# Kernel tuning notes

Measured on AMD Instinct MI355X. Metric: run time of the kernel, lower is better.

## Reference

```python
import jax, jax.numpy as jnp
import numpy as np


def setup_inputs() -> dict:
    key = jax.random.key(0)
    ks = jax.random.split(key, 15)
    B, r, d, h, na = 64, 64, 2048, 64, 256
    x = jax.random.normal(ks[0], (B, d, na), dtype=jnp.float32)
    L = jax.random.randint(ks[1], (B, 2, na), 0, 2).astype(jnp.float32)
    p = lambda i, shp: jax.random.normal(ks[i], shp, dtype=jnp.float32)
    return {
        "x": x, "L": L,
        "Aq": p(2, (r, d)), "Ak": p(3, (r, d)), "Av": p(4, (r, d)),
        "Aq1": p(5, (r, r)), "Ak1": p(6, (r, r)), "Av1": p(7, (r, r)),
        "Aq5": p(8, (r, r)), "Ak5": p(9, (r, r)), "Av5": p(10, (r, r)),
        "Ao": p(11, (r, r)), "Ao1": p(12, (r, r)), "Ao5": p(13, (h, r)),
    }


def reference(x, L, Aq, Ak, Av, Aq1, Ak1, Av1, Aq5, Ak5, Av5, Ao, Ao1, Ao5):
    B, d, na = x.shape
    # numNeighbors: count of L[:,0,:] >= 1 per batch, +1 -> [B,1,1]
    numN = jnp.sum((L[:, 0, :] >= 1.0).astype(jnp.float32), axis=1)[:, None, None] + 1.0
    scale = jnp.sqrt(numN)  # [B,1,1]

    def attn(M, Wq, Wk, Wv):
        # M: [B, f, na]; Wq/Wk/Wv: [r, f]
        Q = jax.nn.sigmoid(jnp.einsum('rf,bfn->bnr', Wq, M))  # [B,na,r]
        K = jax.nn.sigmoid(jnp.einsum('rf,bfn->brn', Wk, M))  # [B,r,na]
        V = jax.nn.sigmoid(jnp.einsum('rf,bfn->bnr', Wv, M))  # [B,na,r]
        A = jax.nn.softmax(jnp.einsum('bnr,brm->bnm', Q, K) / scale, axis=2)
        return jnp.einsum('bnm,bmr->brn', A, V)  # [B,r,na]

    o = attn(x, Aq, Ak, Av)
    M = jax.nn.silu(jnp.einsum('sr,brn->bsn', Ao, o))
    o = attn(M, Aq1, Ak1, Av1)
    M = jax.nn.silu(jnp.einsum('sr,brn->bsn', Ao1, o))
    o = attn(M, Aq5, Ak5, Av5)
    M = jax.nn.silu(jnp.einsum('hr,brn->bhn', Ao5, o))  # [B,h,na]

    blk = d // na  # rows per block (8)
    def diagvec(i):
        # kron(sum-of-squares, ones(1,2)) == repeat each element twice -> [B, 2*na]
        return jnp.repeat(jnp.sum(M[:, i * blk:(i + 1) * blk, :] ** 2, axis=1), 2, axis=1)

    M11, M12, M21, M22 = diagvec(0), diagvec(1), diagvec(2), diagvec(3)
    Mpp = jnp.sum(M[:, 4 * blk:, :] ** 2, axis=1)  # [B, na]

    # q = x[:, :4, :].transpose(1,2).reshape(B, 4*na) (agent-major ordering)
    q = jnp.transpose(x[:, :4, :], (0, 2, 1)).reshape(B, 4 * na)
    q1, q2 = q[:, :2 * na], q[:, 2 * na:]
    # Block matrix [[diag(M11), diag(M12)], [diag(M21), diag(M22)]] quadratic form,
    # computed without materializing the [B, 4na, 4na] matrix.
    quad = jnp.sum(M11 * q1 * q1 + M12 * q1 * q2 + M21 * q2 * q1 + M22 * q2 * q2,
                   axis=1, keepdims=True)
    return quad + jnp.sum(Mpp, axis=1, keepdims=True)  # [B, 1]
```

## Files before the change

### kernel.cpp

```cpp
#include <hip/hip_runtime.h>
#include <stdint.h>

typedef _Float16 f16;
typedef f16 f16x8 __attribute__((ext_vector_type(8)));
typedef float f32x4 __attribute__((ext_vector_type(4)));

#define MFMA(a,b,c) __builtin_amdgcn_mfma_f32_16x16x32_f16(a, b, c, 0, 0, 0)

__device__ __forceinline__ float sigmoidf_(float z) { return 1.0f / (1.0f + __expf(-z)); }

__global__ void prep_kernel(const float* __restrict__ L,
    const float* __restrict__ Aq, const float* __restrict__ Ak, const float* __restrict__ Av,
    const float* __restrict__ Aq1, const float* __restrict__ Ak1, const float* __restrict__ Av1,
    const float* __restrict__ Aq5, const float* __restrict__ Ak5, const float* __restrict__ Av5,
    const float* __restrict__ Ao, const float* __restrict__ Ao1, const float* __restrict__ Ao5,
    float* __restrict__ scale, f16* __restrict__ Wcat, f16* __restrict__ Wsm)
{
  __shared__ float r4[4];
  int blk = blockIdx.x, t = threadIdx.x;
  if (blk < 64) {
    float v = (L[blk * 512 + t] >= 1.0f) ? 1.0f : 0.0f;
    #pragma unroll
    for (int off = 32; off; off >>= 1) v += __shfl_down(v, off);
    if ((t & 63) == 0) r4[t >> 6] = v;
    __syncthreads();
    if (t == 0) scale[blk] = sqrtf(r4[0] + r4[1] + r4[2] + r4[3] + 1.0f);
  } else if (blk < 160) {
    int base = (blk - 64) * 4096;
    for (int i = 0; i < 16; i++) {
      int idx = base + t + i * 256;
      int row = idx >> 11, col = idx & 2047;
      float v = (row < 64) ? Aq[row * 2048 + col]
              : (row < 128) ? Ak[(row - 64) * 2048 + col]
              : Av[(row - 128) * 2048 + col];
      Wcat[idx] = (f16)v;
    }
  } else {
    int j = blk - 160;
    const float* s = (j == 0) ? Aq1 : (j == 1) ? Ak1 : (j == 2) ? Av1 : (j == 3) ? Aq5
                   : (j == 4) ? Ak5 : (j == 5) ? Av5 : (j == 6) ? Ao : (j == 7) ? Ao1 : Ao5;
    for (int i = 0; i < 16; i++) { int idx = t + i * 256; Wsm[j * 4096 + idx] = (f16)s[idx]; }
  }
}

__global__ __launch_bounds__(256) void qkv1_kernel(const float* __restrict__ x,
    const f16* __restrict__ Wcat, f16* __restrict__ Qt, f16* __restrict__ Kt,
    f16* __restrict__ Vg)
{
  int b = blockIdx.y, n0 = blockIdx.x * 64;
  int t = threadIdx.x, lane = t & 63, w = t >> 6;
  int l15 = lane & 15, q = lane >> 4;
  __shared__ f16 xt[64 * 72];
  __shared__ f16 wt[192 * 72];
  f32x4 acc[4][3] = {};
  const float* xb = x + (size_t)b * 2048 * 256 + n0;
  int tn = t & 63, fp0 = t >> 6;

  for (int f0 = 0; f0 < 2048; f0 += 64) {
    #pragma unroll
    for (int rep = 0; rep < 8; rep++) {
      int fl = (fp0 + rep * 4) * 2;
      float a0 = xb[(size_t)(f0 + fl) * 256 + tn];
      float a1 = xb[(size_t)(f0 + fl + 1) * 256 + tn];
      uint32_t pk = (uint32_t)__builtin_bit_cast(uint16_t, (f16)a0)
                  | ((uint32_t)__builtin_bit_cast(uint16_t, (f16)a1) << 16);
      *(uint32_t*)&xt[tn * 72 + fl] = pk;
    }
    #pragma unroll
    for (int i = 0; i < 6; i++) {
      int id = t + i * 256, r = id >> 3, c = id & 7;
      uint4 v = *(const uint4*)(Wcat + (size_t)r * 2048 + f0 + c * 8);
      *(uint4*)&wt[r * 72 + c * 8] = v;
    }
    __syncthreads();
    #pragma unroll
    for (int ks = 0; ks < 2; ks++) {
      int k0 = ks * 32 + q * 8;
      f16x8 af[4], bf[3];
      #pragma unroll
      for (int nt = 0; nt < 4; nt++) af[nt] = *(const f16x8*)&xt[(nt * 16 + l15) * 72 + k0];
      #pragma unroll
      for (int j = 0; j < 3; j++) bf[j] = *(const f16x8*)&wt[((w * 3 + j) * 16 + l15) * 72 + k0];
      #pragma unroll
      for (int nt = 0; nt < 4; nt++)
        #pragma unroll
        for (int j = 0; j < 3; j++)
          acc[nt][j] = MFMA(af[nt], bf[j], acc[nt][j]);
    }
    __syncthreads();
  }
  #pragma unroll
  for (int nt = 0; nt < 4; nt++)
    #pragma unroll
    for (int j = 0; j < 3; j++) {
      int rr = (w * 3 + j) * 16 + l15;
      float s[4];
      #pragma unroll
      for (int reg = 0; reg < 4; reg++) s[reg] = sigmoidf_(acc[nt][j][reg]);
      int nbase = n0 + nt * 16 + q * 4;
      if (rr < 64) {
        #pragma unroll
        for (int reg = 0; reg < 4; reg++)
          Qt[(size_t)b * 16384 + (size_t)(nbase + reg) * 64 + rr] = (f16)s[reg];
      } else if (rr < 128) {
        #pragma unroll
        for (int reg = 0; reg < 4; reg++)
          Kt[(size_t)b * 16384 + (size_t)(nbase + reg) * 64 + (rr - 64)] = (f16)s[reg];
      } else {
        union { f16 h[4]; uint2 u; } pk;
        #pragma unroll
        for (int reg = 0; reg < 4; reg++) pk.h[reg] = (f16)s[reg];
        *(uint2*)(Vg + (size_t)b * 16384 + (size_t)(rr - 128) * 256 + nbase) = pk.u;
      }
    }
}

__global__ __launch_bounds__(512) void attn_kernel(const float* __restrict__ x,
    const float* __restrict__ scale, const f16* __restrict__ Wsm,
    const f16* __restrict__ Qtg, const f16* __restrict__ Ktg, const f16* __restrict__ Vgg,
    float* __restrict__ out)
{
  int b = blockIdx.x;
  int t = threadIdx.x, lane = t & 63, w = t >> 6;
  int l15 = lane & 15, q = lane >> 4;
  __shared__ f16 S1[256 * 72];
  __shared__ f16 S2[256 * 72];
  __shared__ f16 S3[256 * 72];
  __shared__ f16 S4[256 * 72];
  __shared__ f16 S5[64 * 72];
  __shared__ float denomS[256];
  __shared__ float red[8];

  float sinv = 1.0f / scale[b];

  {
    const uint4* qs = (const uint4*)(Qtg + (size_t)b * 16384);
    const uint4* ks = (const uint4*)(Ktg + (size_t)b * 16384);
    const uint4* vs = (const uint4*)(Vgg + (size_t)b * 16384);
    #pragma unroll
    for (int i = 0; i < 4; i++) {
      int id = t + i * 512;
      int n = id >> 3, c = id & 7;
      *(uint4*)((char*)S2 + n * 144 + c * 16) = qs[id];
      *(uint4*)((char*)S3 + n * 144 + c * 16) = ks[id];
    }
    #pragma unroll
    for (int i = 0; i < 4; i++) {
      int id = t + i * 512;
      int r = id >> 5, c = id & 31;
      *(uint4*)((char*)S1 + r * 528 + c * 16) = vs[id];
    }
    if (t < 256) denomS[t] = 0.0f;
  }
  __syncthreads();

  #pragma unroll 1
  for (int l = 0; l < 3; l++) {
    if (l > 0) {
      const f16* Wq = Wsm + (size_t)((l == 1) ? 0 : 3) * 4096;
      const f16* Wk = Wsm + (size_t)((l == 1) ? 1 : 4) * 4096;
      f16x8 bq[4][2], bk[4][2];
      #pragma unroll
      for (int rt = 0; rt < 4; rt++) {
        int r = rt * 16 + l15;
        bq[rt][0] = *(const f16x8*)(Wq + r * 64 + q * 8);
        bq[rt][1] = *(const f16x8*)(Wq + r * 64 + 32 + q * 8);
        bk[rt][0] = *(const f16x8*)(Wk + r * 64 + q * 8);
        bk[rt][1] = *(const f16x8*)(Wk + r * 64 + 32 + q * 8);
      }
      #pragma unroll
      for (int half = 0; half < 2; half++) {
        int nt = 2 * w + half;
        int arow = (nt * 16 + l15) * 72;
        f16x8 af0 = *(const f16x8*)&S1[arow + q * 8];
        f16x8 af1 = *(const f16x8*)&S1[arow + 32 + q * 8];
        #pragma unroll
        for (int rt = 0; rt < 4; rt++) {
          f32x4 aq = {}; aq = MFMA(af0, bq[rt][0], aq); aq = MFMA(af1, bq[rt][1], aq);
          f32x4 akk = {}; akk = MFMA(af0, bk[rt][0], akk); akk = MFMA(af1, bk[rt][1], akk);
          int col = rt * 16 + l15;
          #pragma unroll
          for (int reg = 0; reg < 4; reg++) {
            int n = nt * 16 + q * 4 + reg;
            S2[n * 72 + col] = (f16)sigmoidf_(aq[reg]);
            S3[n * 72 + col] = (f16)sigmoidf_(akk[reg]);
          }
        }
      }
      if (t < 256) denomS[t] = 0.0f;
    }
    __syncthreads();

    f32x4 oacc[2][4] = {};
    const f16* Wv = Wsm + (size_t)((l == 1) ? 2 : 5) * 4096;

    #pragma unroll 1
    for (int ch = 0; ch < 4; ch++) {
      int m0 = ch * 64;
      if (l > 0) {
        #pragma unroll
        for (int i = 0; i < 2; i++) {
          int id = 2 * w + i, rt = id >> 2, mt = id & 3;
          int r = rt * 16 + l15;
          f16x8 a0 = *(const f16x8*)(Wv + r * 64 + q * 8);
          f16x8 a1 = *(const f16x8*)(Wv + r * 64 + 32 + q * 8);
          int brow = (m0 + mt * 16 + l15) * 72;
          f16x8 b0 = *(const f16x8*)&S1[brow + q * 8];
          f16x8 b1 = *(const f16x8*)&S1[brow + 32 + q * 8];
          f32x4 a = {}; a = MFMA(a0, b0, a); a = MFMA(a1, b1, a);
          int col = mt * 16 + l15;
          #pragma unroll
          for (int reg = 0; reg < 4; reg++)
            S5[(rt * 16 + q * 4 + reg) * 72 + col] = (f16)sigmoidf_(a[reg]);
        }
      }
      #pragma unroll
      for (int half = 0; half < 2; half++) {
        int nt = 2 * w + half;
        int arow = (nt * 16 + l15) * 72;
        f16x8 af0 = *(const f16x8*)&S2[arow + q * 8];
        f16x8 af1 = *(const f16x8*)&S2[arow + 32 + q * 8];
        #pragma unroll
        for (int mt = 0; mt < 4; mt++) {
          int brow = (m0 + mt * 16 + l15) * 72;
          f16x8 b0 = *(const f16x8*)&S3[brow + q * 8];
          f16x8 b1 = *(const f16x8*)&S3[brow + 32 + q * 8];
          f32x4 a = {}; a = MFMA(af0, b0, a); a = MFMA(af1, b1, a);
          int col = mt * 16 + l15;
          #pragma unroll
          for (int reg = 0; reg < 4; reg++) {
            float e = __expf(a[reg] * sinv);
            S4[(nt * 16 + q * 4 + reg) * 72 + col] = (f16)e;
          }
        }
      }
      __syncthreads();
      if (t < 256) {
        float s = 0.0f;
        const f16* row = &S4[t * 72];
        #pragma unroll
        for (int jj = 0; jj < 8; jj++) {
          f16x8 v = *(const f16x8*)(row + jj * 8);
          s += (float)v[0] + (float)v[1] + (float)v[2] + (float)v[3]
             + (float)v[4] + (float)v[5] + (float)v[6] + (float)v[7];
        }
        denomS[t] += s;
      }
      {
        f16x8 vb[4][2];
        #pragma unroll
        for (int rt = 0; rt < 4; rt++) {
          int r = rt * 16 + l15;
          if (l == 0) {
            vb[rt][0] = *(const f16x8*)&S1[r * 264 + m0 + q * 8];
            vb[rt][1] = *(const f16x8*)&S1[r * 264 + m0 + 32 + q * 8];
          } else {
            vb[rt][0] = *(const f16x8*)&S5[r * 72 + q * 8];
            vb[rt][1] = *(const f16x8*)&S5[r * 72 + 32 + q * 8];
          }
        }
        #pragma unroll
        for (int half = 0; half < 2; half++) {
          int nt = 2 * w + half;
          int arow = (nt * 16 + l15) * 72;
          f16x8 af0 = *(const f16x8*)&S4[arow + q * 8];
          f16x8 af1 = *(const f16x8*)&S4[arow + 32 + q * 8];
          #pragma unroll
          for (int rt = 0; rt < 4; rt++) {
            oacc[half][rt] = MFMA(af0, vb[rt][0], oacc[half][rt]);
            oacc[half][rt] = MFMA(af1, vb[rt][1], oacc[half][rt]);
          }
        }
      }
      __syncthreads();
    }

    #pragma unroll
    for (int half = 0; half < 2; half++) {
      int nt = 2 * w + half;
      #pragma unroll
      for (int rt = 0; rt < 4; rt++) {
        int col = rt * 16 + l15;
        #pragma unroll
        for (int reg = 0; reg < 4; reg++) {
          int n = nt * 16 + q * 4 + reg;
          S2[n * 72 + col] = (f16)(oacc[half][rt][reg] / denomS[n]);
        }
      }
    }
    __syncthreads();
    {
      const f16* Wo = Wsm + (size_t)((l == 0) ? 6 : (l == 1) ? 7 : 8) * 4096;
      f16x8 bo[4][2];
      #pragma unroll
      for (int st = 0; st < 4; st++) {
        int s = st * 16 + l15;
        bo[st][0] = *(const f16x8*)(Wo + s * 64 + q * 8);
        bo[st][1] = *(const f16x8*)(Wo + s * 64 + 32 + q * 8);
      }
      #pragma unroll
      for (int half = 0; half < 2; half++) {
        int nt = 2 * w + half;
        int arow = (nt * 16 + l15) * 72;
        f16x8 af0 = *(const f16x8*)&S2[arow + q * 8];
        f16x8 af1 = *(const f16x8*)&S2[arow + 32 + q * 8];
        #pragma unroll
        for (int st = 0; st < 4; st++) {
          f32x4 a = {}; a = MFMA(af0, bo[st][0], a); a = MFMA(af1, bo[st][1], a);
          int col = st * 16 + l15;
          #pragma unroll
          for (int reg = 0; reg < 4; reg++) {
            float z = a[reg];
            S1[(nt * 16 + q * 4 + reg) * 72 + col] = (f16)(z * sigmoidf_(z));
          }
        }
      }
    }
    __syncthreads();
  }

  float contrib = 0.0f;
  if (t < 256) {
    int n = t;
    const f16* row = &S1[n * 72];
    float d[4] = {0, 0, 0, 0}, pp = 0.0f;
    #pragma unroll
    for (int g = 0; g < 8; g++) {
      f16x8 v = *(const f16x8*)(row + g * 8);
      float ss = 0.0f;
      #pragma unroll
      for (int k = 0; k < 8; k++) { float f = (float)v[k]; ss += f * f; }
      if (g < 4) d[g] = ss; else pp += ss;
    }
    const float* xb = x + (size_t)b * 524288 + (size_t)((n & 1) * 2) * 256;
    int np = n >> 1;
    float q1a = xb[np], q1b = xb[256 + np];
    float q2a = xb[128 + np], q2b = xb[256 + 128 + np];
    contrib = d[0] * (q1a * q1a + q1b * q1b)
            + (d[1] + d[2]) * (q1a * q2a + q1b * q2b)
            + d[3] * (q2a * q2a + q2b * q2b) + pp;
  }
  #pragma unroll
  for (int off = 32; off; off >>= 1) contrib += __shfl_down(contrib, off);
  if (lane == 0) red[w] = contrib;
  __syncthreads();
  if (t == 0) {
    float s = 0.0f;
    #pragma unroll
    for (int i = 0; i < 8; i++) s += red[i];
    out[b] = s;
  }
}

extern "C" void kernel_launch(void* const* d_in, const int* in_sizes, int n_in,
                              void* d_out, int out_size, void* d_ws, size_t ws_size,
                              hipStream_t stream) {
  const float* x   = (const float*)d_in[0];
  const float* L   = (const float*)d_in[1];
  const float* Aq  = (const float*)d_in[2];
  const float* Ak  = (const float*)d_in[3];
  const float* Av  = (const float*)d_in[4];
  const float* Aq1 = (const float*)d_in[5];
  const float* Ak1 = (const float*)d_in[6];
  const float* Av1 = (const float*)d_in[7];
  const float* Aq5 = (const float*)d_in[8];
  const float* Ak5 = (const float*)d_in[9];
  const float* Av5 = (const float*)d_in[10];
  const float* Ao  = (const float*)d_in[11];
  const float* Ao1 = (const float*)d_in[12];
  const float* Ao5 = (const float*)d_in[13];

  char* ws = (char*)d_ws;
  float* scale = (float*)ws;
  f16* Wcat = (f16*)(ws + 256);
  f16* Wsm  = (f16*)(ws + 256 + 786432);
  f16* Qtg  = (f16*)(ws + 860416);
  f16* Ktg  = (f16*)(ws + 860416 + 2097152);
  f16* Vgg  = (f16*)(ws + 860416 + 2 * 2097152);
  float* out = (float*)d_out;

  prep_kernel<<<169, 256, 0, stream>>>(L, Aq, Ak, Av, Aq1, Ak1, Av1,
                                       Aq5, Ak5, Av5, Ao, Ao1, Ao5, scale, Wcat, Wsm);
  qkv1_kernel<<<dim3(4, 64), 256, 0, stream>>>(x, Wcat, Qtg, Ktg, Vgg);
  attn_kernel<<<64, 512, 0, stream>>>(x, scale, Wsm, Qtg, Ktg, Vgg, out);
}
```

Measured before the change: 294.5 us.

## Split per-batch attention into per-layer kernels tiled over query blocks

The single 64-block attention kernel, which ran all three layers per batch, becomes three templated per-layer kernels launched on a 4x64 grid. Each block handles 64 query tokens and recomputes the full K and V projections from the previous layer's M, which is passed between kernels through global buffers. The final reduction uses an atomicAdd into an output that the prep kernel zeroes. The qkv1 GEMM tile is also halved to launch twice as many blocks. The aim is to fill far more compute units than the 64 used before, at the cost of redundant K/V work, extra launches and global round-trips.

Measured after the change: 272.1 us. 1.08x faster.

```diff
diff --git a/kernel.cpp b/kernel.cpp
--- a/kernel.cpp
+++ b/kernel.cpp
@@ -14,7 +14,8 @@
     const float* __restrict__ Aq1, const float* __restrict__ Ak1, const float* __restrict__ Av1,
     const float* __restrict__ Aq5, const float* __restrict__ Ak5, const float* __restrict__ Av5,
     const float* __restrict__ Ao, const float* __restrict__ Ao1, const float* __restrict__ Ao5,
-    float* __restrict__ scale, f16* __restrict__ Wcat, f16* __restrict__ Wsm)
+    float* __restrict__ scale, f16* __restrict__ Wcat, f16* __restrict__ Wsm,
+    float* __restrict__ out)
 {
   __shared__ float r4[4];
   int blk = blockIdx.x, t = threadIdx.x;
@@ -35,11 +36,13 @@
               : Av[(row - 128) * 2048 + col];
       Wcat[idx] = (f16)v;
     }
-  } else {
+  } else if (blk < 169) {
     int j = blk - 160;
     const float* s = (j == 0) ? Aq1 : (j == 1) ? Ak1 : (j == 2) ? Av1 : (j == 3) ? Aq5
                    : (j == 4) ? Ak5 : (j == 5) ? Av5 : (j == 6) ? Ao : (j == 7) ? Ao1 : Ao5;
     for (int i = 0; i < 16; i++) { int idx = t + i * 256; Wsm[j * 4096 + idx] = (f16)s[idx]; }
+  } else {
+    if (t < 64) out[t] = 0.0f;
   }
 }
 
@@ -47,19 +50,19 @@
     const f16* __restrict__ Wcat, f16* __restrict__ Qt, f16* __restrict__ Kt,
     f16* __restrict__ Vg)
 {
-  int b = blockIdx.y, n0 = blockIdx.x * 64;
+  int b = blockIdx.y, n0 = blockIdx.x * 32;
   int t = threadIdx.x, lane = t & 63, w = t >> 6;
   int l15 = lane & 15, q = lane >> 4;
-  __shared__ f16 xt[64 * 72];
+  __shared__ f16 xt[32 * 72];
   __shared__ f16 wt[192 * 72];
-  f32x4 acc[4][3] = {};
-  const float* xb = x + (size_t)b * 2048 * 256 + n0;
-  int tn = t & 63, fp0 = t >> 6;
+  f32x4 acc[2][3] = {};
+  const float* xb = x + (size_t)b * 524288 + n0;
+  int tn = t & 31, fg = t >> 5;
 
   for (int f0 = 0; f0 < 2048; f0 += 64) {
     #pragma unroll
-    for (int rep = 0; rep < 8; rep++) {
-      int fl = (fp0 + rep * 4) * 2;
+    for (int rep = 0; rep < 4; rep++) {
+      int fl = fg * 8 + rep * 2;
       float a0 = xb[(size_t)(f0 + fl) * 256 + tn];
       float a1 = xb[(size_t)(f0 + fl + 1) * 256 + tn];
       uint32_t pk = (uint32_t)__builtin_bit_cast(uint16_t, (f16)a0)
@@ -69,20 +72,19 @@
     #pragma unroll
     for (int i = 0; i < 6; i++) {
       int id = t + i * 256, r = id >> 3, c = id & 7;
-      uint4 v = *(const uint4*)(Wcat + (size_t)r * 2048 + f0 + c * 8);
-      *(uint4*)&wt[r * 72 + c * 8] = v;
+      *(uint4*)&wt[r * 72 + c * 8] = *(const uint4*)(Wcat + (size_t)r * 2048 + f0 + c * 8);
     }
     __syncthreads();
     #pragma unroll
     for (int ks = 0; ks < 2; ks++) {
       int k0 = ks * 32 + q * 8;
-      f16x8 af[4], bf[3];
-      #pragma unroll
-      for (int nt = 0; nt < 4; nt++) af[nt] = *(const f16x8*)&xt[(nt * 16 + l15) * 72 + k0];
+      f16x8 af[2], bf[3];
+      af[0] = *(const f16x8*)&xt[l15 * 72 + k0];
+      af[1] = *(const f16x8*)&xt[(16 + l15) * 72 + k0];
       #pragma unroll
       for (int j = 0; j < 3; j++) bf[j] = *(const f16x8*)&wt[((w * 3 + j) * 16 + l15) * 72 + k0];
       #pragma unroll
-      for (int nt = 0; nt < 4; nt++)
+      for (int nt = 0; nt < 2; nt++)
         #pragma unroll
         for (int j = 0; j < 3; j++)
           acc[nt][j] = MFMA(af[nt], bf[j], acc[nt][j]);
@@ -90,7 +92,7 @@
     __syncthreads();
   }
   #pragma unroll
-  for (int nt = 0; nt < 4; nt++)
+  for (int nt = 0; nt < 2; nt++)
     #pragma unroll
     for (int j = 0; j < 3; j++) {
       int rr = (w * 3 + j) * 16 + l15;
@@ -115,240 +117,219 @@
     }
 }
 
-__global__ __launch_bounds__(512) void attn_kernel(const float* __restrict__ x,
+template<int LAYER>
+__global__ __launch_bounds__(512) void attnB_kernel(const float* __restrict__ x,
     const float* __restrict__ scale, const f16* __restrict__ Wsm,
     const f16* __restrict__ Qtg, const f16* __restrict__ Ktg, const f16* __restrict__ Vgg,
-    float* __restrict__ out)
+    const f16* __restrict__ Min, f16* __restrict__ Mout, float* __restrict__ out)
 {
-  int b = blockIdx.x;
+  int g = blockIdx.x, b = blockIdx.y, n0 = g * 64;
   int t = threadIdx.x, lane = t & 63, w = t >> 6;
   int l15 = lane & 15, q = lane >> 4;
-  __shared__ f16 S1[256 * 72];
-  __shared__ f16 S2[256 * 72];
-  __shared__ f16 S3[256 * 72];
-  __shared__ f16 S4[256 * 72];
-  __shared__ f16 S5[64 * 72];
-  __shared__ float denomS[256];
-  __shared__ float red[8];
+  __shared__ f16 KT[256 * 72];
+  __shared__ f16 SM[256 * 72];
+  __shared__ f16 VM[64 * 264];
+  __shared__ f16 QT[64 * 72];
+  __shared__ f16 OT[64 * 72];
+  __shared__ float denomS[64];
 
   float sinv = 1.0f / scale[b];
-
-  {
-    const uint4* qs = (const uint4*)(Qtg + (size_t)b * 16384);
+  if (t < 64) denomS[t] = 0.0f;
+
+  if (LAYER == 0) {
+    const uint4* qs = (const uint4*)(Qtg + (size_t)b * 16384 + (size_t)n0 * 64);
+    { int n = t >> 3, c = t & 7; *(uint4*)&QT[n * 72 + c * 8] = qs[t]; }
     const uint4* ks = (const uint4*)(Ktg + (size_t)b * 16384);
     const uint4* vs = (const uint4*)(Vgg + (size_t)b * 16384);
     #pragma unroll
     for (int i = 0; i < 4; i++) {
       int id = t + i * 512;
-      int n = id >> 3, c = id & 7;
-      *(uint4*)((char*)S2 + n * 144 + c * 16) = qs[id];
-      *(uint4*)((char*)S3 + n * 144 + c * 16) = ks[id];
-    }
+      int m = id >> 3, c = id & 7;
+      *(uint4*)&KT[m * 72 + c * 8] = ks[id];
+      int r = id >> 5, c2 = id & 31;
+      *(uint4*)&VM[r * 264 + c2 * 8] = vs[id];
+    }
+  } else {
+    const uint4* ms = (const uint4*)(Min + (size_t)b * 16384);
     #pragma unroll
     for (int i = 0; i < 4; i++) {
-      int id = t + i * 512;
-      int r = id >> 5, c = id & 31;
-      *(uint4*)((char*)S1 + r * 528 + c * 16) = vs[id];
-    }
-    if (t < 256) denomS[t] = 0.0f;
+      int id = t + i * 512, m = id >> 3, c = id & 7;
+      *(uint4*)&SM[m * 72 + c * 8] = ms[id];
+    }
   }
   __syncthreads();
 
-  #pragma unroll 1
-  for (int l = 0; l < 3; l++) {
-    if (l > 0) {
-      const f16* Wq = Wsm + (size_t)((l == 1) ? 0 : 3) * 4096;
-      const f16* Wk = Wsm + (size_t)((l == 1) ? 1 : 4) * 4096;
-      f16x8 bq[4][2], bk[4][2];
+  const f16* Wq = Wsm + (size_t)(LAYER == 1 ? 0 : 3) * 4096;
+  const f16* Wk = Wsm + (size_t)(LAYER == 1 ? 1 : 4) * 4096;
+  const f16* Wv = Wsm + (size_t)(LAYER == 1 ? 2 : 5) * 4096;
+  const f16* Wo = Wsm + (size_t)(LAYER == 0 ? 6 : (LAYER == 1 ? 7 : 8)) * 4096;
+
+  if (LAYER > 0) {
+    if (w < 4) {
+      f16x8 bk[4][2];
       #pragma unroll
       for (int rt = 0; rt < 4; rt++) {
-        int r = rt * 16 + l15;
-        bq[rt][0] = *(const f16x8*)(Wq + r * 64 + q * 8);
-        bq[rt][1] = *(const f16x8*)(Wq + r * 64 + 32 + q * 8);
-        bk[rt][0] = *(const f16x8*)(Wk + r * 64 + q * 8);
-        bk[rt][1] = *(const f16x8*)(Wk + r * 64 + 32 + q * 8);
-      }
-      #pragma unroll
-      for (int half = 0; half < 2; half++) {
-        int nt = 2 * w + half;
-        int arow = (nt * 16 + l15) * 72;
-        f16x8 af0 = *(const f16x8*)&S1[arow + q * 8];
-        f16x8 af1 = *(const f16x8*)&S1[arow + 32 + q * 8];
+        bk[rt][0] = *(const f16x8*)(Wk + (rt * 16 + l15) * 64 + q * 8);
+        bk[rt][1] = *(const f16x8*)(Wk + (rt * 16 + l15) * 64 + 32 + q * 8);
+      }
+      #pragma unroll
+      for (int mi = 0; mi < 4; mi++) {
+        int mt = w * 4 + mi;
+        f16x8 a0 = *(const f16x8*)&SM[(mt * 16 + l15) * 72 + q * 8];
+        f16x8 a1 = *(const f16x8*)&SM[(mt * 16 + l15) * 72 + 32 + q * 8];
         #pragma unroll
         for (int rt = 0; rt < 4; rt++) {
-          f32x4 aq = {}; aq = MFMA(af0, bq[rt][0], aq); aq = MFMA(af1, bq[rt][1], aq);
-          f32x4 akk = {}; akk = MFMA(af0, bk[rt][0], akk); akk = MFMA(af1, bk[rt][1], akk);
-          int col = rt * 16 + l15;
-          #pragma unroll
-          for (int reg = 0; reg < 4; reg++) {
-            int n = nt * 16 + q * 4 + reg;
-            S2[n * 72 + col] = (f16)sigmoidf_(aq[reg]);
-            S3[n * 72 + col] = (f16)sigmoidf_(akk[reg]);
-          }
-        }
-      }
-      if (t < 256) denomS[t] = 0.0f;
-    }
-    __syncthreads();
-
-    f32x4 oacc[2][4] = {};
-    const f16* Wv = Wsm + (size_t)((l == 1) ? 2 : 5) * 4096;
-
-    #pragma unroll 1
-    for (int ch = 0; ch < 4; ch++) {
-      int m0 = ch * 64;
-      if (l > 0) {
-        #pragma unroll
-        for (int i = 0; i < 2; i++) {
-          int id = 2 * w + i, rt = id >> 2, mt = id & 3;
-          int r = rt * 16 + l15;
-          f16x8 a0 = *(const f16x8*)(Wv + r * 64 + q * 8);
-          f16x8 a1 = *(const f16x8*)(Wv + r * 64 + 32 + q * 8);
-          int brow = (m0 + mt * 16 + l15) * 72;
-          f16x8 b0 = *(const f16x8*)&S1[brow + q * 8];
-          f16x8 b1 = *(const f16x8*)&S1[brow + 32 + q * 8];
-          f32x4 a = {}; a = MFMA(a0, b0, a); a = MFMA(a1, b1, a);
-          int col = mt * 16 + l15;
+          f32x4 acc = {}; acc = MFMA(a0, bk[rt][0], acc); acc = MFMA(a1, bk[rt][1], acc);
           #pragma unroll
           for (int reg = 0; reg < 4; reg++)
-            S5[(rt * 16 + q * 4 + reg) * 72 + col] = (f16)sigmoidf_(a[reg]);
+            KT[(mt * 16 + q * 4 + reg) * 72 + rt * 16 + l15] = (f16)sigmoidf_(acc[reg]);
         }
       }
-      #pragma unroll
-      for (int half = 0; half < 2; half++) {
-        int nt = 2 * w + half;
-        int arow = (nt * 16 + l15) * 72;
-        f16x8 af0 = *(const f16x8*)&S2[arow + q * 8];
-        f16x8 af1 = *(const f16x8*)&S2[arow + 32 + q * 8];
-        #pragma unroll
-        for (int mt = 0; mt < 4; mt++) {
-          int brow = (m0 + mt * 16 + l15) * 72;
-          f16x8 b0 = *(const f16x8*)&S3[brow + q * 8];
-          f16x8 b1 = *(const f16x8*)&S3[brow + 32 + q * 8];
-          f32x4 a = {}; a = MFMA(af0, b0, a); a = MFMA(af1, b1, a);
-          int col = mt * 16 + l15;
+    } else {
+      f16x8 av[4][2];
+      #pragma unroll
+      for (int rt = 0; rt < 4; rt++) {
+        av[rt][0] = *(const f16x8*)(Wv + (rt * 16 + l15) * 64 + q * 8);
+        av[rt][1] = *(const f16x8*)(Wv + (rt * 16 + l15) * 64 + 32 + q * 8);
+      }
+      #pragma unroll
+      for (int mi = 0; mi < 4; mi++) {
+        int mt = (w - 4) * 4 + mi;
+        f16x8 b0 = *(const f16x8*)&SM[(mt * 16 + l15) * 72 + q * 8];
+        f16x8 b1 = *(const f16x8*)&SM[(mt * 16 + l15) * 72 + 32 + q * 8];
+        #pragma unroll
+        for (int rt = 0; rt < 4; rt++) {
+          f32x4 acc = {}; acc = MFMA(av[rt][0], b0, acc); acc = MFMA(av[rt][1], b1, acc);
           #pragma unroll
-          for (int reg = 0; reg < 4; reg++) {
-            float e = __expf(a[reg] * sinv);
-            S4[(nt * 16 + q * 4 + reg) * 72 + col] = (f16)e;
-          }
+          for (int reg = 0; reg < 4; reg++)
+            VM[(rt * 16 + q * 4 + reg) * 264 + mt * 16 + l15] = (f16)sigmoidf_(acc[reg]);
         }
       }
-      __syncthreads();
-      if (t < 256) {
-        float s = 0.0f;
-        const f16* row = &S4[t * 72];
-        #pragma unroll
-        for (int jj = 0; jj < 8; jj++) {
-          f16x8 v = *(const f16x8*)(row + jj * 8);
-          s += (float)v[0] + (float)v[1] + (float)v[2] + (float)v[3]
-             + (float)v[4] + (float)v[5] + (float)v[6] + (float)v[7];
-        }
-        denomS[t] += s;
-      }
-      {
-        f16x8 vb[4][2];
-        #pragma unroll
-        for (int rt = 0; rt < 4; rt++) {
-          int r = rt * 16 + l15;
-          if (l == 0) {
-            vb[rt][0] = *(const f16x8*)&S1[r * 264 + m0 + q * 8];
-            vb[rt][1] = *(const f16x8*)&S1[r * 264 + m0 + 32 + q * 8];
-          } else {
-            vb[rt][0] = *(const f16x8*)&S5[r * 72 + q * 8];
-            vb[rt][1] = *(const f16x8*)&S5[r * 72 + 32 + q * 8];
-          }
-        }
-        #pragma unroll
-        for (int half = 0; half < 2; half++) {
-          int nt = 2 * w + half;
-          int arow = (nt * 16 + l15) * 72;
-          f16x8 af0 = *(const f16x8*)&S4[arow + q * 8];
-          f16x8 af1 = *(const f16x8*)&S4[arow + 32 + q * 8];
-          #pragma unroll
-          for (int rt = 0; rt < 4; rt++) {
-            oacc[half][rt] = MFMA(af0, vb[rt][0], oacc[half][rt]);
-            oacc[half][rt] = MFMA(af1, vb[rt][1], oacc[half][rt]);
-          }
-        }
-      }
-      __syncthreads();
-    }
-
-    #pragma unroll
-    for (int half = 0; half < 2; half++) {
-      int nt = 2 * w + half;
-      #pragma unroll
-      for (int rt = 0; rt < 4; rt++) {
-        int col = rt * 16 + l15;
-        #pragma unroll
-        for (int reg = 0; reg < 4; reg++) {
-          int n = nt * 16 + q * 4 + reg;
-          S2[n * 72 + col] = (f16)(oacc[half][rt][reg] / denomS[n]);
-        }
+    }
+    {
+      int nt = w >> 1;
+      f16x8 a0 = *(const f16x8*)&SM[(n0 + nt * 16 + l15) * 72 + q * 8];
+      f16x8 a1 = *(const f16x8*)&SM[(n0 + nt * 16 + l15) * 72 + 32 + q * 8];
+      #pragma unroll
+      for (int j = 0; j < 2; j++) {
+        int rt = (w & 1) * 2 + j;
+        f16x8 b0 = *(const f16x8*)(Wq + (rt * 16 + l15) * 64 + q * 8);
+        f16x8 b1 = *(const f16x8*)(Wq + (rt * 16 + l15) * 64 + 32 + q * 8);
+        f32x4 acc = {}; acc = MFMA(a0, b0, acc); acc = MFMA(a1, b1, acc);
+        #pragma unroll
+        for (int reg = 0; reg < 4; reg++)
+          QT[(nt * 16 + q * 4 + reg) * 72 + rt * 16 + l15] = (f16)sigmoidf_(acc[reg]);
       }
     }
     __syncthreads();
-    {
-      const f16* Wo = Wsm + (size_t)((l == 0) ? 6 : (l == 1) ? 7 : 8) * 4096;
-      f16x8 bo[4][2];
-      #pragma unroll
-      for (int st = 0; st < 4; st++) {
-        int s = st * 16 + l15;
-        bo[st][0] = *(const f16x8*)(Wo + s * 64 + q * 8);
-        bo[st][1] = *(const f16x8*)(Wo + s * 64 + 32 + q * 8);
-      }
-      #pragma unroll
-      for (int half = 0; half < 2; half++) {
-        int nt = 2 * w + half;
-        int arow = (nt * 16 + l15) * 72;
-        f16x8 af0 = *(const f16x8*)&S2[arow + q * 8];
-        f16x8 af1 = *(const f16x8*)&S2[arow + 32 + q * 8];
-        #pragma unroll
-        for (int st = 0; st < 4; st++) {
-          f32x4 a = {}; a = MFMA(af0, bo[st][0], a); a = MFMA(af1, bo[st][1], a);
-          int col = st * 16 + l15;
-          #pragma unroll
-          for (int reg = 0; reg < 4; reg++) {
-            float z = a[reg];
-            S1[(nt * 16 + q * 4 + reg) * 72 + col] = (f16)(z * sigmoidf_(z));
-          }
-        }
-      }
-    }
-    __syncthreads();
-  }
-
-  float contrib = 0.0f;
-  if (t < 256) {
-    int n = t;
-    const f16* row = &S1[n * 72];
-    float d[4] = {0, 0, 0, 0}, pp = 0.0f;
-    #pragma unroll
-    for (int g = 0; g < 8; g++) {
-      f16x8 v = *(const f16x8*)(row + g * 8);
-      float ss = 0.0f;
-      #pragma unroll
-      for (int k = 0; k < 8; k++) { float f = (float)v[k]; ss += f * f; }
-      if (g < 4) d[g] = ss; else pp += ss;
-    }
-    const float* xb = x + (size_t)b * 524288 + (size_t)((n & 1) * 2) * 256;
-    int np = n >> 1;
-    float q1a = xb[np], q1b = xb[256 + np];
-    float q2a = xb[128 + np], q2b = xb[256 + 128 + np];
-    contrib = d[0] * (q1a * q1a + q1b * q1b)
-            + (d[1] + d[2]) * (q1a * q2a + q1b * q2b)
-            + d[3] * (q2a * q2a + q2b * q2b) + pp;
-  }
-  #pragma unroll
-  for (int off = 32; off; off >>= 1) contrib += __shfl_down(contrib, off);
-  if (lane == 0) red[w] = contrib;
+  }
+
+  {
+    int nt = w >> 1;
+    f16x8 a0 = *(const f16x8*)&QT[(nt * 16 + l15) * 72 + q * 8];
+    f16x8 a1 = *(const f16x8*)&QT[(nt * 16 + l15) * 72 + 32 + q * 8];
+    float dsum[4] = {0.f, 0.f, 0.f, 0.f};
+    #pragma unroll
+    for (int mi = 0; mi < 8; mi++) {
+      int mt = (w & 1) * 8 + mi;
+      f16x8 b0 = *(const f16x8*)&KT[(mt * 16 + l15) * 72 + q * 8];
+      f16x8 b1 = *(const f16x8*)&KT[(mt * 16 + l15) * 72 + 32 + q * 8];
+      f32x4 acc = {}; acc = MFMA(a0, b0, acc); acc = MFMA(a1, b1, acc);
+      #pragma unroll
+      for (int reg = 0; reg < 4; reg++) {
+        float e = __expf(acc[reg] * sinv);
+        dsum[reg] += e;
+        SM[(nt * 16 + q * 4 + reg) * 264 + mt * 16 + l15] = (f16)e;
+      }
+    }
+    #pragma unroll
+    for (int reg = 0; reg < 4; reg++) {
+      #pragma unroll
+      for (int mask = 1; mask < 16; mask <<= 1) dsum[reg] += __shfl_xor(dsum[reg], mask);
+    }
+    if (l15 == 0) {
+      #pragma unroll
+      for (int reg = 0; reg < 4; reg++) atomicAdd(&denomS[nt * 16 + q * 4 + reg], dsum[reg]);
+    }
+  }
   __syncthreads();
-  if (t == 0) {
-    float s = 0.0f;
-    #pragma unroll
-    for (int i = 0; i < 8; i++) s += red[i];
-    out[b] = s;
+
+  {
+    int nt = w >> 1;
+    f32x4 oacc[2] = {};
+    #pragma unroll
+    for (int kc = 0; kc < 8; kc++) {
+      f16x8 af = *(const f16x8*)&SM[(nt * 16 + l15) * 264 + kc * 32 + q * 8];
+      #pragma unroll
+      for (int j = 0; j < 2; j++) {
+        int rt = (w & 1) * 2 + j;
+        f16x8 bf = *(const f16x8*)&VM[(rt * 16 + l15) * 264 + kc * 32 + q * 8];
+        oacc[j] = MFMA(af, bf, oacc[j]);
+      }
+    }
+    #pragma unroll
+    for (int j = 0; j < 2; j++) {
+      int rt = (w & 1) * 2 + j;
+      #pragma unroll
+      for (int reg = 0; reg < 4; reg++) {
+        int row = nt * 16 + q * 4 + reg;
+        OT[row * 72 + rt * 16 + l15] = (f16)(oacc[j][reg] / denomS[row]);
+      }
+    }
+  }
+  __syncthreads();
+
+  f16* Mst = QT;
+  {
+    int nt = w >> 1;
+    f16x8 a0 = *(const f16x8*)&OT[(nt * 16 + l15) * 72 + q * 8];
+    f16x8 a1 = *(const f16x8*)&OT[(nt * 16 + l15) * 72 + 32 + q * 8];
+    #pragma unroll
+    for (int j = 0; j < 2; j++) {
+      int st = (w & 1) * 2 + j;
+      f16x8 b0 = *(const f16x8*)(Wo + (st * 16 + l15) * 64 + q * 8);
+      f16x8 b1 = *(const f16x8*)(Wo + (st * 16 + l15) * 64 + 32 + q * 8);
+      f32x4 acc = {}; acc = MFMA(a0, b0, acc); acc = MFMA(a1, b1, acc);
+      #pragma unroll
+      for (int reg = 0; reg < 4; reg++) {
+        float z = acc[reg];
+        Mst[(nt * 16 + q * 4 + reg) * 64 + st * 16 + l15] = (f16)(z * sigmoidf_(z));
+      }
+    }
+  }
+  __syncthreads();
+
+  if (LAYER < 2) {
+    int row = t >> 3, c = t & 7;
+    *(uint4*)(Mout + (size_t)b * 16384 + (size_t)(n0 + row) * 64 + c * 8)
+        = *(const uint4*)&Mst[row * 64 + c * 8];
+  } else {
+    float contrib = 0.0f;
+    if (t < 64) {
+      int ntok = n0 + t;
+      const f16* row = &Mst[t * 64];
+      float d[4] = {0, 0, 0, 0}, pp = 0.0f;
+      #pragma unroll
+      for (int gg = 0; gg < 8; gg++) {
+        f16x8 v = *(const f16x8*)(row + gg * 8);
+        float ss = 0.0f;
+        #pragma unroll
+        for (int k = 0; k < 8; k++) { float f = (float)v[k]; ss += f * f; }
+        if (gg < 4) d[gg] = ss; else pp += ss;
+      }
+      int np = ntok >> 1, c0 = (ntok & 1) * 2;
+      const float* xb = x + (size_t)b * 524288 + (size_t)c0 * 256;
+      float q1a = xb[np], q1b = xb[256 + np];
+      float q2a = xb[128 + np], q2b = xb[384 + np];
+      contrib = d[0] * (q1a * q1a + q1b * q1b)
+              + (d[1] + d[2]) * (q1a * q2a + q1b * q2b)
+              + d[3] * (q2a * q2a + q2b * q2b) + pp;
+    }
+    if (w == 0) {
+      #pragma unroll
+      for (int off = 32; off; off >>= 1) contrib += __shfl_down(contrib, off);
+      if (lane == 0) atomicAdd(out + b, contrib);
+    }
   }
 }
 
@@ -372,15 +353,22 @@
 
   char* ws = (char*)d_ws;
   float* scale = (float*)ws;
-  f16* Wcat = (f16*)(ws + 256);
-  f16* Wsm  = (f16*)(ws + 256 + 786432);
-  f16* Qtg  = (f16*)(ws + 860416);
-  f16* Ktg  = (f16*)(ws + 860416 + 2097152);
-  f16* Vgg  = (f16*)(ws + 860416 + 2 * 2097152);
+  f16* Wcat  = (f16*)(ws + 256);
+  f16* Wsm   = (f16*)(ws + 786688);
+  f16* Qtg   = (f16*)(ws + 860416);
+  f16* Ktg   = (f16*)(ws + 2957568);
+  f16* Vgg   = (f16*)(ws + 5054720);
+  f16* MbufA = (f16*)(ws + 7151872);
+  f16* MbufB = (f16*)(ws + 9249024);
   float* out = (float*)d_out;
 
-  prep_kernel<<<169, 256, 0, stream>>>(L, Aq, Ak, Av, Aq1, Ak1, Av1,
-                                       Aq5, Ak5, Av5, Ao, Ao1, Ao5, scale, Wcat, Wsm);
-  qkv1_kernel<<<dim3(4, 64), 256, 0, stream>>>(x, Wcat, Qtg, Ktg, Vgg);
-  attn_kernel<<<64, 512, 0, stream>>>(x, scale, Wsm, Qtg, Ktg, Vgg, out);
+  prep_kernel<<<170, 256, 0, stream>>>(L, Aq, Ak, Av, Aq1, Ak1, Av1,
+                                       Aq5, Ak5, Av5, Ao, Ao1, Ao5, scale, Wcat, Wsm, out);
+  qkv1_kernel<<<dim3(8, 64), 256, 0, stream>>>(x, Wcat, Qtg, Ktg, Vgg);
+  attnB_kernel<0><<<dim3(4, 64), 512, 0, stream>>>(x, scale, Wsm, Qtg, Ktg, Vgg,
+                                                   nullptr, MbufA, out);
+  attnB_kernel<1><<<dim3(4, 64), 512, 0, stream>>>(x, scale, Wsm, Qtg, Ktg, Vgg,
+                                                   MbufA, MbufB, out);
+  attnB_kernel<2><<<dim3(4, 64), 512, 0, stream>>>(x, scale, Wsm, Qtg, Ktg, Vgg,
+                                                   MbufB, nullptr, out);
 }
```
